# Performance work log

Hardware: AMD Instinct MI355X
Metric: run time of the kernel (lower is better)

The kernel has to match this reference:

```python
import jax, jax.numpy as jnp
import numpy as np

B, T, D = 4, 2048, 1024
H = 16
HD = D // H  # 64

def setup_inputs() -> dict:
    key = jax.random.key(0)
    k1, k2, k3 = jax.random.split(key, 3)
    x = jax.random.normal(k1, (B, T, D), dtype=jnp.float32)
    # torch nn.Linear weight layout: [out_features, in_features]
    w_qkv = jax.random.normal(k2, (3 * D, D), dtype=jnp.float32) * (D ** -0.5)
    w_proj = jax.random.normal(k3, (D, D), dtype=jnp.float32) * (D ** -0.5)
    return {"x": x, "w_qkv": w_qkv, "w_proj": w_proj}

def reference(x, w_qkv, w_proj):
    b, t, c = x.shape
    qkv = jnp.einsum('btc,oc->bto', x, w_qkv)  # [b,t,3c]
    q, k, v = jnp.split(qkv, 3, axis=-1)
    # [b,h,t,hd]
    q = q.reshape(b, t, H, HD).transpose(0, 2, 1, 3)
    k = k.reshape(b, t, H, HD).transpose(0, 2, 1, 3)
    v = v.reshape(b, t, H, HD).transpose(0, 2, 1, 3)
    att = jnp.einsum('bhqd,bhkd->bhqk', q, k) / (HD ** 0.5)
    causal = jnp.tril(jnp.ones((t, t), dtype=bool))
    att = jnp.where(causal, att, -jnp.inf)
    att = jax.nn.softmax(att, axis=-1)
    y = jnp.einsum('bhqk,bhkd->bhqd', att, v)
    y = y.transpose(0, 2, 1, 3).reshape(b, t, c)
    return jnp.einsum('btc,oc->bto', y, w_proj)
```

## Files before the change

### kernel.cpp

```cpp
#include <hip/hip_runtime.h>
#include <cstdint>
#include <cstddef>


typedef __bf16 bf16;
typedef __bf16 bf16x4 __attribute__((ext_vector_type(4)));
typedef __bf16 bf16x8 __attribute__((ext_vector_type(8)));
typedef float  f32x4  __attribute__((ext_vector_type(4)));
typedef float  fvec4  __attribute__((ext_vector_type(4)));
typedef unsigned u32x2 __attribute__((ext_vector_type(2)));

typedef __attribute__((address_space(1))) const void global_cv;
typedef __attribute__((address_space(3))) void lds_v;

#define MFMA16(a, b, c) __builtin_amdgcn_mfma_f32_16x16x32_bf16((a), (b), (c), 0, 0, 0)

#define QSCALE 0.18033688f

__device__ __forceinline__ void async_ld16(const bf16* g, bf16* l) {
  __builtin_amdgcn_global_load_lds((global_cv*)g, (lds_v*)l, 16, 0, 0);
}

__device__ __forceinline__ int swz_off(int row, int col) {
  int sr = (row & 7) ^ ((row >> 3) & 7);
  return row * 64 + ((((col >> 3) ^ sr) & 7) * 8) + (col & 7);
}

__device__ __forceinline__ unsigned cvt_pk(float lo, float hi) {
  unsigned r;
  asm("v_cvt_pk_bf16_f32 %0, %1, %2" : "=v"(r) : "v"(lo), "v"(hi));
  return r;
}

__device__ __forceinline__ bf16x8 cvt8(const float* p) {
  fvec4 u = *(const fvec4*)p;
  fvec4 v = *(const fvec4*)(p + 4);
  bf16x8 r;
  r[0] = (bf16)u[0]; r[1] = (bf16)u[1]; r[2] = (bf16)u[2]; r[3] = (bf16)u[3];
  r[4] = (bf16)v[0]; r[5] = (bf16)v[1]; r[6] = (bf16)v[2]; r[7] = (bf16)v[3];
  return r;
}

__global__ void cvt_all(const float* __restrict__ x, const float* __restrict__ wq,
                        const float* __restrict__ wp, bf16* __restrict__ xb,
                        bf16* __restrict__ wqb, bf16* __restrict__ wpb) {
  int i = blockIdx.x * 256 + threadIdx.x;
  const float* s;
  bf16* d;
  int off;
  if (i < 1048576)      { s = x;  d = xb;  off = i; }
  else if (i < 1441792) { s = wq; d = wqb; off = i - 1048576; }
  else                  { s = wp; d = wpb; off = i - 1441792; }
  *(bf16x8*)(d + (size_t)off * 8) = cvt8(s + (size_t)off * 8);
}

__device__ __forceinline__ void qkv_scatter(const f32x4 acc[4][4], int m0, int n0,
                                            int wm, int wn, int quad, int l15,
                                            bf16* Qo, bf16* Ko, bf16* Vo) {
  const int which = n0 >> 10;
  if (which == 2) {
#pragma unroll
    for (int i = 0; i < 4; ++i) {
      const int m = m0 + wm + i * 16 + quad * 4;
      const int b = m >> 11;
      const int t = m & 2047;
#pragma unroll
      for (int j = 0; j < 4; ++j) {
        const int n1 = (n0 + wn + j * 16 + l15) & 1023;
        const int h  = n1 >> 6;
        const int d  = n1 & 63;
        bf16x4 v;
#pragma unroll
        for (int r = 0; r < 4; ++r) v[r] = (bf16)acc[i][j][r];
        *(bf16x4*)(Vo + ((size_t)(b * 16 + h) * 64 + d) * 2048 + t) = v;
      }
    }
    return;
  }
  bf16* dst = (which == 0) ? Qo : Ko;
  const float scale = (which == 0) ? QSCALE : 1.0f;
#pragma unroll
  for (int i = 0; i < 4; ++i) {
    const int m = m0 + wm + i * 16 + quad * 4;
#pragma unroll
    for (int j = 0; j < 4; ++j) {
      const int n  = n0 + wn + j * 16 + l15;
      const int n1 = n & 1023;
      const int h  = n1 >> 6;
      const int d  = n1 & 63;
#pragma unroll
      for (int r = 0; r < 4; ++r) {
        const int mm = m + r;
        const int b  = mm >> 11;
        const int t  = mm & 2047;
        dst[(((size_t)(b * 16 + h)) * 2048 + t) * 64 + d] =
            (bf16)(acc[i][j][r] * scale);
      }
    }
  }
}

__global__ __launch_bounds__(256, 2)
void gemm_qkv_a(const bf16* __restrict__ A, const bf16* __restrict__ B,
                bf16* __restrict__ Qo, bf16* __restrict__ Ko,
                bf16* __restrict__ Vo) {
  __shared__ __align__(16) bf16 As[2][128 * 32];
  __shared__ __align__(16) bf16 Bs[2][128 * 32];
  const int K = 1024;

  const int tid  = threadIdx.x;
  const int lane = tid & 63;
  const int wave = tid >> 6;
  const int quad = lane >> 4;
  const int l15  = lane & 15;
  const int wm   = (wave >> 1) * 64;
  const int wn   = (wave & 1) * 64;

  const int lin = (int)blockIdx.x + (int)blockIdx.y * 24;
  const int xcd = lin & 7;
  const int sl  = lin >> 3;
  const int n0  = (xcd * 3 + (sl % 3)) * 128;
  const int m0  = (sl / 3) * 128;

  f32x4 acc[4][4];
#pragma unroll
  for (int i = 0; i < 4; ++i)
#pragma unroll
    for (int j = 0; j < 4; ++j) acc[i][j] = f32x4{0.f, 0.f, 0.f, 0.f};

  const int r0 = tid >> 2;
  const int c0 = (tid & 3) * 8;
  const bf16* ag0 = A + (size_t)(m0 + r0) * K + c0;
  const bf16* ag1 = A + (size_t)(m0 + 64 + r0) * K + c0;
  const bf16* bg0 = B + (size_t)(n0 + r0) * K + c0;
  const bf16* bg1 = B + (size_t)(n0 + 64 + r0) * K + c0;
  const int lo0 = (wave * 64) * 8;
  const int lo1 = (256 + wave * 64) * 8;

  async_ld16(ag0, As[0] + lo0);
  async_ld16(ag1, As[0] + lo1);
  async_ld16(bg0, Bs[0] + lo0);
  async_ld16(bg1, Bs[0] + lo1);
  __syncthreads();

  for (int it = 0; it < 32; ++it) {
    const int cur = it & 1;
    if (it < 31) {
      const int kn = (it + 1) * 32;
      async_ld16(ag0 + kn, As[cur ^ 1] + lo0);
      async_ld16(ag1 + kn, As[cur ^ 1] + lo1);
      async_ld16(bg0 + kn, Bs[cur ^ 1] + lo0);
      async_ld16(bg1 + kn, Bs[cur ^ 1] + lo1);
    }

    bf16x8 af[4], bfr[4];
#pragma unroll
    for (int i = 0; i < 4; ++i)
      af[i] = *(const bf16x8*)(As[cur] + (wm + i * 16 + l15) * 32 + quad * 8);
#pragma unroll
    for (int j = 0; j < 4; ++j)
      bfr[j] = *(const bf16x8*)(Bs[cur] + (wn + j * 16 + l15) * 32 + quad * 8);
#pragma unroll
    for (int i = 0; i < 4; ++i)
#pragma unroll
      for (int j = 0; j < 4; ++j)
        acc[i][j] = MFMA16(af[i], bfr[j], acc[i][j]);

    __syncthreads();
  }
  qkv_scatter(acc, m0, n0, wm, wn, quad, l15, Qo, Ko, Vo);
}

__global__ __launch_bounds__(256, 2)
void gemm_qkv_f(const float* __restrict__ A, const float* __restrict__ B,
                bf16* __restrict__ Qo, bf16* __restrict__ Ko,
                bf16* __restrict__ Vo) {
  __shared__ __align__(16) bf16 As[128 * 32];
  __shared__ __align__(16) bf16 Bs[128 * 32];
  const int K = 1024;

  const int tid  = threadIdx.x;
  const int lane = tid & 63;
  const int wave = tid >> 6;
  const int quad = lane >> 4;
  const int l15  = lane & 15;
  const int wm   = (wave >> 1) * 64;
  const int wn   = (wave & 1) * 64;

  const int lin = (int)blockIdx.x + (int)blockIdx.y * 24;
  const int xcd = lin & 7;
  const int sl  = lin >> 3;
  const int n0  = (xcd * 3 + (sl % 3)) * 128;
  const int m0  = (sl / 3) * 128;

  f32x4 acc[4][4];
#pragma unroll
  for (int i = 0; i < 4; ++i)
#pragma unroll
    for (int j = 0; j < 4; ++j) acc[i][j] = f32x4{0.f, 0.f, 0.f, 0.f};

  const int r0 = tid >> 2;
  const int c0 = (tid & 3) * 8;
  const size_t aoff0 = (size_t)(m0 + r0) * K + c0;
  const size_t aoff1 = (size_t)(m0 + 64 + r0) * K + c0;
  const size_t boff0 = (size_t)(n0 + r0) * K + c0;
  const size_t boff1 = (size_t)(n0 + 64 + r0) * K + c0;

  for (int k0 = 0; k0 < K; k0 += 32) {
    bf16x8 va0 = cvt8(A + aoff0 + k0);
    bf16x8 va1 = cvt8(A + aoff1 + k0);
    bf16x8 vb0 = cvt8(B + boff0 + k0);
    bf16x8 vb1 = cvt8(B + boff1 + k0);
    __syncthreads();
    *(bf16x8*)(As + tid * 8)        = va0;
    *(bf16x8*)(As + 2048 + tid * 8) = va1;
    *(bf16x8*)(Bs + tid * 8)        = vb0;
    *(bf16x8*)(Bs + 2048 + tid * 8) = vb1;
    __syncthreads();

    bf16x8 af[4], bfr[4];
#pragma unroll
    for (int i = 0; i < 4; ++i)
      af[i] = *(const bf16x8*)(As + (wm + i * 16 + l15) * 32 + quad * 8);
#pragma unroll
    for (int j = 0; j < 4; ++j)
      bfr[j] = *(const bf16x8*)(Bs + (wn + j * 16 + l15) * 32 + quad * 8);
#pragma unroll
    for (int i = 0; i < 4; ++i)
#pragma unroll
      for (int j = 0; j < 4; ++j)
        acc[i][j] = MFMA16(af[i], bfr[j], acc[i][j]);
  }
  qkv_scatter(acc, m0, n0, wm, wn, quad, l15, Qo, Ko, Vo);
}

__global__ __launch_bounds__(256, 4)
void attn(const bf16* __restrict__ Q, const bf16* __restrict__ Kk,
          const bf16* __restrict__ Vt, bf16* __restrict__ Y) {
  __shared__ __align__(16) bf16 Ks[2][64 * 64];
  __shared__ __align__(16) bf16 Vs[2][64 * 64];
  __shared__ __align__(16) bf16 Ps[4 * 16 * 64];

  const int tid  = threadIdx.x;
  const int wave = tid >> 6;
  const int lane = tid & 63;
  const int quad = lane >> 4;
  const int l15  = lane & 15;

  const int lin  = (int)blockIdx.x + ((int)blockIdx.y << 4);
  const int slot = lin >> 3;
  const int bh   = (lin & 7) * 8 + (slot >> 4);
  const int p    = slot & 15;
  const int b    = bh >> 4;
  const int h    = bh & 15;

  const bf16* Qb = Q  + (size_t)bh * (2048 * 64);
  const bf16* Kb = Kk + (size_t)bh * (2048 * 64);
  const bf16* Vb = Vt + (size_t)bh * (2048 * 64);
  char* Pw = (char*)(Ps + wave * (16 * 64));

  const int r0s = wave * 8 + (lane >> 3);
  const int r1s = r0s + 32;
  const int qch = lane & 7;
  const int co0 = (((qch ^ ((r0s & 7) ^ ((r0s >> 3) & 7)))) & 7) * 8;
  const int co1 = (((qch ^ ((r1s & 7) ^ ((r1s >> 3) & 7)))) & 7) * 8;
  const bf16* kg0 = Kb + (size_t)r0s * 64 + co0;
  const bf16* kg1 = Kb + (size_t)r1s * 64 + co1;
  const bf16* vg0 = Vb + (size_t)r0s * 2048 + co0;
  const bf16* vg1 = Vb + (size_t)r1s * 2048 + co1;
  const int ldsw = wave * 512;

  const int psx   = l15 & 7;
  const int prowb = l15 * 128;
  const int pr0   = prowb + ((quad ^ psx) << 4);
  const int pr1   = prowb + (((4 + quad) ^ psx) << 4);

  const float NEG = -1e30f;

#pragma unroll 1
  for (int pass = 0; pass < 2; ++pass) {
    const int qt = pass ? (31 - p) : p;
    const int q0 = qt * 64;

    const bf16* qp = Qb + (size_t)(q0 + wave * 16 + l15) * 64 + quad * 8;
    bf16x8 qa0 = *(const bf16x8*)qp;
    bf16x8 qa1 = *(const bf16x8*)(qp + 32);

    f32x4 l4 = {0.f, 0.f, 0.f, 0.f};
    f32x4 o[4];
#pragma unroll
    for (int j = 0; j < 4; ++j) o[j] = f32x4{0.f, 0.f, 0.f, 0.f};

    async_ld16(kg0, Ks[0] + ldsw);
    async_ld16(kg1, Ks[0] + 2048 + ldsw);
    async_ld16(vg0, Vs[0] + ldsw);
    async_ld16(vg1, Vs[0] + 2048 + ldsw);
    __syncthreads();

#pragma unroll 1
    for (int kt = 0; kt <= qt; ++kt) {
      const int cur = kt & 1;
      const int k0  = kt * 64;

      if (kt < qt) {
        const int kn = k0 + 64;
        async_ld16(kg0 + (size_t)kn * 64, Ks[cur ^ 1] + ldsw);
        async_ld16(kg1 + (size_t)kn * 64, Ks[cur ^ 1] + 2048 + ldsw);
        async_ld16(vg0 + kn, Vs[cur ^ 1] + ldsw);
        async_ld16(vg1 + kn, Vs[cur ^ 1] + 2048 + ldsw);
      }

      f32x4 s[4];
      __builtin_amdgcn_s_setprio(1);
#pragma unroll
      for (int j = 0; j < 4; ++j) {
        const int kvr = j * 16 + l15;
        bf16x8 k0f = *(const bf16x8*)(Ks[cur] + swz_off(kvr, quad * 8));
        bf16x8 k1f = *(const bf16x8*)(Ks[cur] + swz_off(kvr, 32 + quad * 8));
        f32x4 z = {0.f, 0.f, 0.f, 0.f};
        z = MFMA16(k0f, qa0, z);
        z = MFMA16(k1f, qa1, z);
        s[j] = z;
      }
      __builtin_amdgcn_s_setprio(0);

      if (kt == qt) {
        const int qloc = wave * 16 + l15;
#pragma unroll
        for (int j = 0; j < 4; ++j) {
#pragma unroll
          for (int r = 0; r < 4; ++r) {
            if (16 * j + 4 * quad + r > qloc) s[j][r] = NEG;
          }
        }
      }

#pragma unroll
      for (int j = 0; j < 4; ++j) {
#pragma unroll
        for (int r = 0; r < 4; ++r) s[j][r] = exp2f(s[j][r]);
        l4 += s[j];
      }

#pragma unroll
      for (int j = 0; j < 4; ++j) {
        u32x2 pk;
        pk[0] = cvt_pk(s[j][0], s[j][1]);
        pk[1] = cvt_pk(s[j][2], s[j][3]);
        const int C = 2 * j + (quad >> 1);
        *(u32x2*)(Pw + prowb + (((C ^ psx) << 4) | ((quad & 1) << 3))) = pk;
      }

      bf16x8 pf0 = *(const bf16x8*)(Pw + pr0);
      bf16x8 pf1 = *(const bf16x8*)(Pw + pr1);

      __builtin_amdgcn_s_setprio(1);
#pragma unroll
      for (int j = 0; j < 4; ++j) {
        const int d = j * 16 + l15;
        bf16x8 vf0 = *(const bf16x8*)(Vs[cur] + swz_off(d, quad * 8));
        bf16x8 vf1 = *(const bf16x8*)(Vs[cur] + swz_off(d, 32 + quad * 8));
        o[j] = MFMA16(pf0, vf0, o[j]);
        o[j] = MFMA16(pf1, vf1, o[j]);
      }
      __builtin_amdgcn_s_setprio(0);

      __syncthreads();
    }

    float lf = (l4[0] + l4[1]) + (l4[2] + l4[3]);
    lf += __shfl_xor(lf, 16);
    lf += __shfl_xor(lf, 32);
    float inv[4];
#pragma unroll
    for (int r = 0; r < 4; ++r) inv[r] = 1.0f / __shfl(lf, quad * 4 + r);

#pragma unroll
    for (int j = 0; j < 4; ++j) {
      const int dcol = h * 64 + j * 16 + l15;
#pragma unroll
      for (int r = 0; r < 4; ++r) {
        const int trow = q0 + wave * 16 + quad * 4 + r;
        Y[((size_t)b * 2048 + trow) * 1024 + dcol] = (bf16)(o[j][r] * inv[r]);
      }
    }
  }
}

__global__ __launch_bounds__(256, 2)
void gemm_proj_a(const bf16* __restrict__ A, const bf16* __restrict__ B,
                 float* __restrict__ C) {
  __shared__ __align__(16) bf16 As[2][128 * 32];
  __shared__ __align__(16) bf16 Bs[2][128 * 32];
  const int K = 1024, N = 1024;

  const int tid  = threadIdx.x;
  const int lane = tid & 63;
  const int wave = tid >> 6;
  const int quad = lane >> 4;
  const int l15  = lane & 15;
  const int wm   = (wave >> 1) * 64;
  const int wn   = (wave & 1) * 64;

  const int lin = (int)blockIdx.x + (int)blockIdx.y * 8;
  const int xcd = lin & 7;
  const int sl  = lin >> 3;
  const int m0  = (xcd * 8 + (sl & 7)) * 128;
  const int n0  = (sl >> 3) * 128;

  f32x4 acc[4][4];
#pragma unroll
  for (int i = 0; i < 4; ++i)
#pragma unroll
    for (int j = 0; j < 4; ++j) acc[i][j] = f32x4{0.f, 0.f, 0.f, 0.f};

  const int r0 = tid >> 2;
  const int c0 = (tid & 3) * 8;
  const bf16* ag0 = A + (size_t)(m0 + r0) * K + c0;
  const bf16* ag1 = A + (size_t)(m0 + 64 + r0) * K + c0;
  const bf16* bg0 = B + (size_t)(n0 + r0) * K + c0;
  const bf16* bg1 = B + (size_t)(n0 + 64 + r0) * K + c0;
  const int lo0 = (wave * 64) * 8;
  const int lo1 = (256 + wave * 64) * 8;

  async_ld16(ag0, As[0] + lo0);
  async_ld16(ag1, As[0] + lo1);
  async_ld16(bg0, Bs[0] + lo0);
  async_ld16(bg1, Bs[0] + lo1);
  __syncthreads();

  for (int it = 0; it < 32; ++it) {
    const int cur = it & 1;
    if (it < 31) {
      const int kn = (it + 1) * 32;
      async_ld16(ag0 + kn, As[cur ^ 1] + lo0);
      async_ld16(ag1 + kn, As[cur ^ 1] + lo1);
      async_ld16(bg0 + kn, Bs[cur ^ 1] + lo0);
      async_ld16(bg1 + kn, Bs[cur ^ 1] + lo1);
    }

    bf16x8 af[4], bfr[4];
#pragma unroll
    for (int i = 0; i < 4; ++i)
      af[i] = *(const bf16x8*)(As[cur] + (wm + i * 16 + l15) * 32 + quad * 8);
#pragma unroll
    for (int j = 0; j < 4; ++j)
      bfr[j] = *(const bf16x8*)(Bs[cur] + (wn + j * 16 + l15) * 32 + quad * 8);
#pragma unroll
    for (int i = 0; i < 4; ++i)
#pragma unroll
      for (int j = 0; j < 4; ++j)
        acc[i][j] = MFMA16(af[i], bfr[j], acc[i][j]);

    __syncthreads();
  }

#pragma unroll
  for (int i = 0; i < 4; ++i) {
    const int m = m0 + wm + i * 16 + quad * 4;
#pragma unroll
    for (int j = 0; j < 4; ++j) {
      const int n = n0 + wn + j * 16 + l15;
#pragma unroll
      for (int r = 0; r < 4; ++r)
        C[(size_t)(m + r) * N + n] = acc[i][j][r];
    }
  }
}

__global__ __launch_bounds__(256, 2)
void gemm_proj_f(const bf16* __restrict__ A, const float* __restrict__ B,
                 float* __restrict__ C) {
  __shared__ __align__(16) bf16 As[128 * 32];
  __shared__ __align__(16) bf16 Bs[128 * 32];
  const int K = 1024, N = 1024;

  const int tid  = threadIdx.x;
  const int lane = tid & 63;
  const int wave = tid >> 6;
  const int quad = lane >> 4;
  const int l15  = lane & 15;
  const int wm   = (wave >> 1) * 64;
  const int wn   = (wave & 1) * 64;

  const int lin = (int)blockIdx.x + (int)blockIdx.y * 8;
  const int xcd = lin & 7;
  const int sl  = lin >> 3;
  const int m0  = (xcd * 8 + (sl & 7)) * 128;
  const int n0  = (sl >> 3) * 128;

  f32x4 acc[4][4];
#pragma unroll
  for (int i = 0; i < 4; ++i)
#pragma unroll
    for (int j = 0; j < 4; ++j) acc[i][j] = f32x4{0.f, 0.f, 0.f, 0.f};

  const int r0 = tid >> 2;
  const int c0 = (tid & 3) * 8;
  const size_t aoff0 = (size_t)(m0 + r0) * K + c0;
  const size_t aoff1 = (size_t)(m0 + 64 + r0) * K + c0;
  const size_t boff0 = (size_t)(n0 + r0) * K + c0;
  const size_t boff1 = (size_t)(n0 + 64 + r0) * K + c0;

  for (int k0 = 0; k0 < K; k0 += 32) {
    bf16x8 va0 = *(const bf16x8*)(A + aoff0 + k0);
    bf16x8 va1 = *(const bf16x8*)(A + aoff1 + k0);
    bf16x8 vb0 = cvt8(B + boff0 + k0);
    bf16x8 vb1 = cvt8(B + boff1 + k0);
    __syncthreads();
    *(bf16x8*)(As + tid * 8)        = va0;
    *(bf16x8*)(As + 2048 + tid * 8) = va1;
    *(bf16x8*)(Bs + tid * 8)        = vb0;
    *(bf16x8*)(Bs + 2048 + tid * 8) = vb1;
    __syncthreads();

    bf16x8 af[4], bfr[4];
#pragma unroll
    for (int i = 0; i < 4; ++i)
      af[i] = *(const bf16x8*)(As + (wm + i * 16 + l15) * 32 + quad * 8);
#pragma unroll
    for (int j = 0; j < 4; ++j)
      bfr[j] = *(const bf16x8*)(Bs + (wn + j * 16 + l15) * 32 + quad * 8);
#pragma unroll
    for (int i = 0; i < 4; ++i)
#pragma unroll
      for (int j = 0; j < 4; ++j)
        acc[i][j] = MFMA16(af[i], bfr[j], acc[i][j]);
  }

#pragma unroll
  for (int i = 0; i < 4; ++i) {
    const int m = m0 + wm + i * 16 + quad * 4;
#pragma unroll
    for (int j = 0; j < 4; ++j) {
      const int n = n0 + wn + j * 16 + l15;
#pragma unroll
      for (int r = 0; r < 4; ++r)
        C[(size_t)(m + r) * N + n] = acc[i][j][r];
    }
  }
}

extern "C" void kernel_launch(void* const* d_in, const int* in_sizes, int n_in,
                              void* d_out, int out_size, void* d_ws, size_t ws_size,
                              hipStream_t stream) {
  const float* x  = nullptr;
  const float* wq = nullptr;
  const float* wp = nullptr;
  for (int i = 0; i < n_in; ++i) {
    if      (in_sizes[i] == 8388608) x  = (const float*)d_in[i];
    else if (in_sizes[i] == 3145728) wq = (const float*)d_in[i];
    else if (in_sizes[i] == 1048576) wp = (const float*)d_in[i];
  }
  if (!x || !wq || !wp) {
    x = (const float*)d_in[0]; wq = (const float*)d_in[1]; wp = (const float*)d_in[2];
  }

  float* out = (float*)d_out;
  const size_t NE = (size_t)4 * 16 * 2048 * 64;
  bf16* kb = (bf16*)d_ws;
  bf16* vb = kb + NE;
  bf16* qb = vb + NE;
  bf16* yb = qb + NE;
  bf16* xb  = yb + NE;
  bf16* wqb = xb + 8388608;
  bf16* wpb = wqb + 3145728;
  const size_t need = (4 * NE + 8388608 + 3145728 + 1048576) * sizeof(bf16);
  const bool ext = ws_size >= need;

  if (ext) {
    cvt_all<<<6144, 256, 0, stream>>>(x, wq, wp, xb, wqb, wpb);
    gemm_qkv_a<<<dim3(24, 64), 256, 0, stream>>>(xb, wqb, qb, kb, vb);
  } else {
    gemm_qkv_f<<<dim3(24, 64), 256, 0, stream>>>(x, wq, qb, kb, vb);
  }

  attn<<<dim3(16, 64), 256, 0, stream>>>(qb, kb, vb, yb);

  if (ext) {
    gemm_proj_a<<<dim3(8, 64), 256, 0, stream>>>(yb, wpb, out);
  } else {
    gemm_proj_f<<<dim3(8, 64), 256, 0, stream>>>(yb, wp, out);
  }
}
```

Measured before the change: 257.0 us.

## Raise GEMM occupancy, simplify LDS addressing, use raw v_exp in attention

Measured after the change: 241.6 us. -6.0%, faster.

```diff
diff --git a/kernel.cpp b/kernel.cpp
--- a/kernel.cpp
+++ b/kernel.cpp
@@ -29,6 +29,12 @@
 __device__ __forceinline__ unsigned cvt_pk(float lo, float hi) {
   unsigned r;
   asm("v_cvt_pk_bf16_f32 %0, %1, %2" : "=v"(r) : "v"(lo), "v"(hi));
+  return r;
+}
+
+__device__ __forceinline__ float exp2_fast(float x) {
+  float r;
+  asm("v_exp_f32 %0, %1" : "=v"(r) : "v"(x));
   return r;
 }
 
@@ -100,12 +106,12 @@
   }
 }
 
-__global__ __launch_bounds__(256, 2)
+__global__ __launch_bounds__(256, 3)
 void gemm_qkv_a(const bf16* __restrict__ A, const bf16* __restrict__ B,
                 bf16* __restrict__ Qo, bf16* __restrict__ Ko,
                 bf16* __restrict__ Vo) {
-  __shared__ __align__(16) bf16 As[2][128 * 32];
-  __shared__ __align__(16) bf16 Bs[2][128 * 32];
+  __shared__ __align__(16) bf16 As[2 * 128 * 32];
+  __shared__ __align__(16) bf16 Bs[2 * 128 * 32];
   const int K = 1024;
 
   const int tid  = threadIdx.x;
@@ -137,29 +143,34 @@
   const int lo0 = (wave * 64) * 8;
   const int lo1 = (256 + wave * 64) * 8;
 
-  async_ld16(ag0, As[0] + lo0);
-  async_ld16(ag1, As[0] + lo1);
-  async_ld16(bg0, Bs[0] + lo0);
-  async_ld16(bg1, Bs[0] + lo1);
+  const int afb = (wm + l15) * 64 + quad * 16;
+  const int bfb = (wn + l15) * 64 + quad * 16;
+
+  async_ld16(ag0, As + lo0);
+  async_ld16(ag1, As + lo1);
+  async_ld16(bg0, Bs + lo0);
+  async_ld16(bg1, Bs + lo1);
+  ag0 += 32; ag1 += 32; bg0 += 32; bg1 += 32;
   __syncthreads();
 
   for (int it = 0; it < 32; ++it) {
     const int cur = it & 1;
     if (it < 31) {
-      const int kn = (it + 1) * 32;
-      async_ld16(ag0 + kn, As[cur ^ 1] + lo0);
-      async_ld16(ag1 + kn, As[cur ^ 1] + lo1);
-      async_ld16(bg0 + kn, Bs[cur ^ 1] + lo0);
-      async_ld16(bg1 + kn, Bs[cur ^ 1] + lo1);
-    }
-
+      const int nb = (cur ^ 1) << 12;
+      async_ld16(ag0, As + nb + lo0);
+      async_ld16(ag1, As + nb + lo1);
+      async_ld16(bg0, Bs + nb + lo0);
+      async_ld16(bg1, Bs + nb + lo1);
+      ag0 += 32; ag1 += 32; bg0 += 32; bg1 += 32;
+    }
+
+    const char* pA = (const char*)As + (cur << 13) + afb;
+    const char* pB = (const char*)Bs + (cur << 13) + bfb;
     bf16x8 af[4], bfr[4];
 #pragma unroll
-    for (int i = 0; i < 4; ++i)
-      af[i] = *(const bf16x8*)(As[cur] + (wm + i * 16 + l15) * 32 + quad * 8);
-#pragma unroll
-    for (int j = 0; j < 4; ++j)
-      bfr[j] = *(const bf16x8*)(Bs[cur] + (wn + j * 16 + l15) * 32 + quad * 8);
+    for (int i = 0; i < 4; ++i) af[i] = *(const bf16x8*)(pA + i * 1024);
+#pragma unroll
+    for (int j = 0; j < 4; ++j) bfr[j] = *(const bf16x8*)(pB + j * 1024);
 #pragma unroll
     for (int i = 0; i < 4; ++i)
 #pragma unroll
@@ -338,7 +349,7 @@
 #pragma unroll
       for (int j = 0; j < 4; ++j) {
 #pragma unroll
-        for (int r = 0; r < 4; ++r) s[j][r] = exp2f(s[j][r]);
+        for (int r = 0; r < 4; ++r) s[j][r] = exp2_fast(s[j][r]);
         l4 += s[j];
       }
 
@@ -387,11 +398,11 @@
   }
 }
 
-__global__ __launch_bounds__(256, 2)
+__global__ __launch_bounds__(256, 3)
 void gemm_proj_a(const bf16* __restrict__ A, const bf16* __restrict__ B,
                  float* __restrict__ C) {
-  __shared__ __align__(16) bf16 As[2][128 * 32];
-  __shared__ __align__(16) bf16 Bs[2][128 * 32];
+  __shared__ __align__(16) bf16 As[2 * 128 * 32];
+  __shared__ __align__(16) bf16 Bs[2 * 128 * 32];
   const int K = 1024, N = 1024;
 
   const int tid  = threadIdx.x;
@@ -423,29 +434,34 @@
   const int lo0 = (wave * 64) * 8;
   const int lo1 = (256 + wave * 64) * 8;
 
-  async_ld16(ag0, As[0] + lo0);
-  async_ld16(ag1, As[0] + lo1);
-  async_ld16(bg0, Bs[0] + lo0);
-  async_ld16(bg1, Bs[0] + lo1);
+  const int afb = (wm + l15) * 64 + quad * 16;
+  const int bfb = (wn + l15) * 64 + quad * 16;
+
+  async_ld16(ag0, As + lo0);
+  async_ld16(ag1, As + lo1);
+  async_ld16(bg0, Bs + lo0);
+  async_ld16(bg1, Bs + lo1);
+  ag0 += 32; ag1 += 32; bg0 += 32; bg1 += 32;
   __syncthreads();
 
   for (int it = 0; it < 32; ++it) {
     const int cur = it & 1;
     if (it < 31) {
-      const int kn = (it + 1) * 32;
-      async_ld16(ag0 + kn, As[cur ^ 1] + lo0);
-      async_ld16(ag1 + kn, As[cur ^ 1] + lo1);
-      async_ld16(bg0 + kn, Bs[cur ^ 1] + lo0);
-      async_ld16(bg1 + kn, Bs[cur ^ 1] + lo1);
-    }
-
+      const int nb = (cur ^ 1) << 12;
+      async_ld16(ag0, As + nb + lo0);
+      async_ld16(ag1, As + nb + lo1);
+      async_ld16(bg0, Bs + nb + lo0);
+      async_ld16(bg1, Bs + nb + lo1);
+      ag0 += 32; ag1 += 32; bg0 += 32; bg1 += 32;
+    }
+
+    const char* pA = (const char*)As + (cur << 13) + afb;
+    const char* pB = (const char*)Bs + (cur << 13) + bfb;
     bf16x8 af[4], bfr[4];
 #pragma unroll
-    for (int i = 0; i < 4; ++i)
-      af[i] = *(const bf16x8*)(As[cur] + (wm + i * 16 + l15) * 32 + quad * 8);
-#pragma unroll
-    for (int j = 0; j < 4; ++j)
-      bfr[j] = *(const bf16x8*)(Bs[cur] + (wn + j * 16 + l15) * 32 + quad * 8);
+    for (int i = 0; i < 4; ++i) af[i] = *(const bf16x8*)(pA + i * 1024);
+#pragma unroll
+    for (int j = 0; j < 4; ++j) bfr[j] = *(const bf16x8*)(pB + j * 1024);
 #pragma unroll
     for (int i = 0; i < 4; ++i)
 #pragma unroll
```
